# Kernel tuning notes

Measured on AMD Instinct MI355X. Metric: run time of the kernel, lower is better.

## Reference

```python
import jax, jax.numpy as jnp
import numpy as np
import math

B, H, W = 4, 224, 224
NFEAT = 2048
N_SP, N_FAM, N_ORD = 200, 38, 13
THRESH = 0.5


def _conv(x, w, b, s):
    y = jax.lax.conv_general_dilated(x, w, (s, s), 'SAME', dimension_numbers=('NCHW', 'OIHW', 'NCHW'))
    return y + b[None, :, None, None]


def _features(x, bw1, bb1, bw2, bb2, bw3, bb3, bw4, bb4):
    # stride-32 CNN backbone standing in for nn.Sequential(*model.children()[:-2]) (2048-ch output)
    x = jax.nn.relu(_conv(x, bw1, bb1, 4))
    x = jax.nn.relu(_conv(x, bw2, bb2, 2))
    x = jax.nn.relu(_conv(x, bw3, bb3, 2))
    x = jax.nn.relu(_conv(x, bw4, bb4, 2))
    return x


def _resize_ac(img, y1, y2, x1, x2, oh, ow):
    # bilinear, align_corners=True resample of img[:, y1:y2, x1:x2] -> (C, oh, ow); jit-safe (gather, no dynamic shapes)
    Hh, Ww = img.shape[1], img.shape[2]
    ys = y1 + jnp.arange(oh, dtype=jnp.float32) * (y2 - 1 - y1) / (oh - 1)
    xs = x1 + jnp.arange(ow, dtype=jnp.float32) * (x2 - 1 - x1) / (ow - 1)
    ylo = jnp.clip(jnp.floor(ys).astype(jnp.int32), 0, Hh - 1)
    yhi = jnp.clip(ylo + 1, 0, Hh - 1)
    yf = (ys - ylo)[None, :, None]
    rows = img[:, ylo, :] * (1 - yf) + img[:, yhi, :] * yf
    xlo = jnp.clip(jnp.floor(xs).astype(jnp.int32), 0, Ww - 1)
    xhi = jnp.clip(xlo + 1, 0, Ww - 1)
    xf = (xs - xlo)[None, None, :]
    return rows[:, :, xlo] * (1 - xf) + rows[:, :, xhi] * xf


def _obj_loc(score, threshold):
    # vectorized, sync-free version of the torch obj_loc interval search
    n = score.shape[0]
    minsize = int(math.ceil(n * 0.125))
    defmax = int(math.ceil(n * 0.875))
    snorm = jnp.sign(score - threshold)
    cross = jnp.abs(snorm[1:] - snorm[:-1]) == 2  # crossing between j and j+1 -> index j+1 starts... torch puts index j in next interval
    ind = jnp.concatenate([cross, jnp.zeros((1,), bool)]).astype(jnp.int32)
    seg = jnp.cumsum(ind)  # segment id per position; matches torch half-open intervals [p_i, p_{i+1})
    k = jnp.sum(ind)       # number of crossings
    idx = jnp.arange(n, dtype=jnp.int32)
    seg_max = jax.ops.segment_max(score, seg, num_segments=n)
    seg_len = jax.ops.segment_sum(jnp.ones((n,), jnp.int32), seg, num_segments=n)
    seg_start = jax.ops.segment_min(idx, seg, num_segments=n)
    seg_end = jax.ops.segment_max(idx, seg, num_segments=n) + 1
    valid = (idx <= k) & (seg_len > 0)
    # torch processing order: first interval, then last, then interiors; ties keep earlier-processed
    order = jnp.where(idx == 0, 0, jnp.where(idx == k, 1, idx + 1))
    m = jnp.where(valid, seg_max, -jnp.inf)
    c1 = valid & (m == jnp.max(m))
    best_len = jnp.max(jnp.where(c1, seg_len, -1))
    c2 = c1 & (seg_len == best_len)
    sel = jnp.argmin(jnp.where(c2, order, n + 2))
    zmin, zmax = seg_start[sel], seg_end[sel]
    # min-size padding, exactly mirroring the sequential torch ifs
    pad = minsize - (zmax - zmin)
    hp = (pad + 1) // 2  # ceil(pad/2)
    need = (zmax - zmin) <= minsize
    cA = need & (zmin > hp) & (n - zmax > pad)
    zmin = jnp.where(cA, zmin - hp + 1, zmin)
    zmax = jnp.where(cA, zmax + hp, zmax)
    cB = need & (zmin < hp)
    zmin = jnp.where(cB, 0, zmin)
    zmax = jnp.where(cB, minsize, zmax)
    cC = need & (n - zmax < hp)
    zmin = jnp.where(cC, n - minsize + 1, zmin)
    zmax = jnp.where(cC, n, zmax)
    # no crossings -> fixed central window (torch early return)
    zmin = jnp.where(k == 0, minsize, zmin)
    zmax = jnp.where(k == 0, defmax, zmax)
    return zmin, zmax


def _norm01(v):
    mn, mx = v.min(), v.max()
    den = jnp.where(mx == mn, mx, mx - mn)
    num = jnp.where(mx == mn, v, v - mn)
    return num / den


def _w_h(gs, wscore, hscore, inputs, threshold):
    def one(g, wsc, hsc, img):
        top = jnp.argmax(g)  # == sort(descending)[0]
        x1, x2 = _obj_loc(_norm01(wsc[top]), threshold)
        y1, y2 = _obj_loc(_norm01(hsc[top]), threshold)
        return _resize_ac(img, y1, y2, x1, x2, img.shape[1], img.shape[2])
    return jax.vmap(one)(gs, wscore, hscore, inputs)


def _stage(gvec, fmap, inputs, wc, bc, wc1, bc1, lf_prev, bb):
    gf = gvec @ wc.T + bc  # conv1x1 on pooled feature == linear
    cam = jax.nn.sigmoid(jnp.einsum('bchw,oc->bohw', jax.lax.stop_gradient(fmap), wc) + bc[None, :, None, None])
    fh, fw = fmap.shape[2], fmap.shape[3]
    cam_up = jax.vmap(lambda im: _resize_ac(im, 0, fh, 0, fw, H, W))(cam)  # (B,C,H,W)
    wsc = cam_up.max(axis=2)  # max_pool2d((h,1)) -> (B,C,W)
    hsc = cam_up.max(axis=3)  # max_pool2d((1,w)) -> (B,C,H)
    lin = _w_h(gf, wsc, hsc, inputs, THRESH)
    la = _features(jax.lax.stop_gradient(lin), *bb)
    lf = la.mean(axis=(2, 3))  # AdaptiveAvgPool2d(1)
    ls = lf @ wc1.T + bc1
    if lf_prev is not None:
        ls = ls + (lf_prev @ wc1.T + bc1)  # bias added twice, as in torch
    return (gf + ls) / 2.0, lf


def _forward(inputs, bw1, bb1, bw2, bb2, bw3, bb3, bw4, bb4, w_ord, b_ord, w_ord1, b_ord1, w_fam, b_fam, w_fam1, b_fam1, w_sp, b_sp, w_sp1, b_sp1):
    bb = (bw1, bb1, bw2, bb2, bw3, bb3, bw4, bb4)
    fmap = _features(inputs, *bb)
    gvec = fmap.mean(axis=(2, 3))
    f_ord, lf_ord = _stage(gvec, fmap, inputs, w_ord, b_ord, w_ord1, b_ord1, None, bb)
    f_fam, lf_fam = _stage(gvec, fmap, inputs, w_fam, b_fam, w_fam1, b_fam1, lf_ord, bb)
    f_sp, _ = _stage(gvec, fmap, inputs, w_sp, b_sp, w_sp1, b_sp1, lf_fam, bb)
    return f_sp, f_fam, f_ord


def setup_inputs() -> dict:
    ks = jax.random.split(jax.random.key(0), 16)
    def he(k, shape, fan_in):
        return jax.random.normal(k, shape, jnp.float32) * np.float32(np.sqrt(2.0 / fan_in))
    d = {"inputs": jax.random.normal(ks[0], (B, 3, H, W), jnp.float32)}
    d["bw1"], d["bb1"] = he(ks[1], (256, 3, 7, 7), 3 * 49), jnp.zeros((256,), jnp.float32)
    d["bw2"], d["bb2"] = he(ks[2], (512, 256, 3, 3), 256 * 9), jnp.zeros((512,), jnp.float32)
    d["bw3"], d["bb3"] = he(ks[3], (1024, 512, 1, 1), 512), jnp.zeros((1024,), jnp.float32)
    d["bw4"], d["bb4"] = he(ks[4], (2048, 1024, 1, 1), 1024), jnp.zeros((2048,), jnp.float32)
    for i, (nm, nc) in enumerate([("ord", N_ORD), ("fam", N_FAM), ("sp", N_SP)]):
        d["w_" + nm] = he(ks[5 + 2 * i], (nc, NFEAT), NFEAT)
        d["b_" + nm] = jnp.zeros((nc,), jnp.float32)
        d["w_" + nm + "1"] = he(ks[6 + 2 * i], (nc, NFEAT), NFEAT)
        d["b_" + nm + "1"] = jnp.zeros((nc,), jnp.float32)
    return d


def reference(inputs, bw1, bb1, bw2, bb2, bw3, bb3, bw4, bb4, w_ord, b_ord, w_ord1, b_ord1, w_fam, b_fam, w_fam1, b_fam1, w_sp, b_sp, w_sp1, b_sp1):
    return _forward(inputs, bw1, bb1, bw2, bb2, bw3, bb3, bw4, bb4, w_ord, b_ord, w_ord1, b_ord1, w_fam, b_fam, w_fam1, b_fam1, w_sp, b_sp, w_sp1, b_sp1)
```

## Files before the change

### kernel.cpp

```cpp
#include <hip/hip_runtime.h>
#include <hip/hip_bf16.h>
#include <math.h>

#define TPB 256

typedef __attribute__((ext_vector_type(8))) short s16x8;
typedef __attribute__((ext_vector_type(8))) unsigned short u16x8;
typedef __attribute__((ext_vector_type(4))) float f32x4;

__global__ void conv3x3s2_k(const float* __restrict__ in, const float* __restrict__ w,
                            const float* __restrict__ bias, float* __restrict__ out, int N)
{
  int bid = blockIdx.x;
  if (N == 4) {
    const int xcd = bid & 7;
    const int n_img = xcd >> 1;
    const int kk = ((bid >> 3) << 1) | (xcd & 1);
    bid = n_img * 392 + kk;
  }
  int idx = bid * blockDim.x + threadIdx.x;
  int total = N * 512 * 28 * 7;
  if (idx >= total) return;
  int oxg = idx % 7; int t = idx / 7; int oy = t % 28; t /= 28; int oc = t % 512; int n = t / 512;
  const float* inp = in + (size_t)n * 256 * 3136;
  const float* wp = w + (size_t)oc * 2304;
  float b0 = bias[oc];
  float acc0 = b0, acc1 = b0, acc2 = b0, acc3 = b0;
  int xb0 = oxg * 8;
  #pragma unroll 4
  for (int ic = 0; ic < 256; ic++) {
    const float* ich = inp + (size_t)ic * 3136;
    const float* wr = wp + ic * 9;
    #pragma unroll
    for (int ky = 0; ky < 3; ky++) {
      int iy = oy * 2 + ky;
      if (iy >= 56) continue;
      const float* row = ich + iy * 56;
      float w0 = wr[ky * 3 + 0], w1 = wr[ky * 3 + 1], w2 = wr[ky * 3 + 2];
      {
        int xb = xb0 + 0;
        acc0 += row[xb] * w0 + row[xb + 1] * w1 + row[xb + 2] * w2;
      }
      {
        int xb = xb0 + 2;
        acc1 += row[xb] * w0 + row[xb + 1] * w1 + row[xb + 2] * w2;
      }
      {
        int xb = xb0 + 4;
        acc2 += row[xb] * w0 + row[xb + 1] * w1 + row[xb + 2] * w2;
      }
      {
        int xb = xb0 + 6;
        acc3 += row[xb] * w0 + row[xb + 1] * w1;
        if (xb + 2 < 56) acc3 += row[xb + 2] * w2;
      }
    }
  }
  float* op = out + (((size_t)n * 512 + oc) * 28 + oy) * 28 + oxg * 4;
  op[0] = fmaxf(acc0, 0.f);
  op[1] = fmaxf(acc1, 0.f);
  op[2] = fmaxf(acc2, 0.f);
  op[3] = fmaxf(acc3, 0.f);
}

template<int KH, int KW, int STRIDE, int PADL, bool BINIT>
__global__ __launch_bounds__(256)
void conv_igemm_k(const float* __restrict__ in, const float* __restrict__ w,
                  const float* __restrict__ bias, float* __restrict__ out,
                  int Cin, int Cout, int Hin, int OH, int Np, int K)
{
  __shared__ float As[16][136];
  __shared__ float Bs[16][64];

  const int tid = threadIdx.x;
  const int bx = blockIdx.x;
  const int by = blockIdx.y;
  const int OHW = OH * OH;
  const int HinHin = Hin * Hin;

  const int n_sub = tid & 63;
  const int kq = tid >> 6;
  const int n_g = bx * 64 + n_sub;
  const bool nvalid = (n_g < Np);
  const int n_c = nvalid ? n_g : 0;
  const int img = n_c / OHW;
  const int p = n_c - img * OHW;
  const int oy = p / OH;
  const int ox = p - oy * OH;
  const int iy0 = oy * STRIDE - PADL;
  const int ix0 = ox * STRIDE - PADL;
  const float* inb = in + (size_t)img * Cin * HinHin;

  const int ks = tid & 15;
  const int msq = tid >> 4;
  const int m_base = by * 128;

  const int m0 = (tid >> 4) * 8;
  const int n0 = (tid & 15) * 4;

  float acc[8][4];
  #pragma unroll
  for (int i = 0; i < 8; i++) {
    const float init = BINIT ? bias[m_base + m0 + i] : 0.f;
    #pragma unroll
    for (int j = 0; j < 4; j++) acc[i][j] = init;
  }

  const int KT = (K + 15) >> 4;
  for (int kt = 0; kt < KT; kt++) {
    const int k0 = kt * 16;
    #pragma unroll
    for (int j = 0; j < 8; j++) {
      const int m = msq + 16 * j;
      const int k = k0 + ks;
      float v = 0.f;
      if (k < K) v = w[(size_t)(m_base + m) * K + k];
      As[ks][m] = v;
    }
    #pragma unroll
    for (int j = 0; j < 4; j++) {
      const int k = k0 + kq * 4 + j;
      float v = 0.f;
      if (nvalid && k < K) {
        const int c = k / (KH * KW);
        const int r = k - c * (KH * KW);
        const int ky = r / KW;
        const int kx = r - ky * KW;
        const int iy = iy0 + ky;
        const int ix = ix0 + kx;
        if (iy >= 0 && iy < Hin && ix >= 0 && ix < Hin)
          v = inb[(size_t)c * HinHin + iy * Hin + ix];
      }
      Bs[kq * 4 + j][n_sub] = v;
    }
    __syncthreads();
    #pragma unroll
    for (int k = 0; k < 16; k++) {
      float a_[8], b_[4];
      #pragma unroll
      for (int i = 0; i < 8; i++) a_[i] = As[k][m0 + i];
      #pragma unroll
      for (int j = 0; j < 4; j++) b_[j] = Bs[k][n0 + j];
      #pragma unroll
      for (int i = 0; i < 8; i++)
        #pragma unroll
        for (int j = 0; j < 4; j++) acc[i][j] += a_[i] * b_[j];
    }
    __syncthreads();
  }

  #pragma unroll
  for (int i = 0; i < 8; i++) {
    const int m = m_base + m0 + i;
    const float bv = BINIT ? 0.f : bias[m];
    #pragma unroll
    for (int j = 0; j < 4; j++) {
      const int nn = bx * 64 + n0 + j;
      if (nn < Np) {
        const int img2 = nn / OHW;
        const int pp = nn - img2 * OHW;
        const float v = BINIT ? acc[i][j] : (acc[i][j] + bv);
        out[((size_t)img2 * Cout + m) * OHW + pp] = fmaxf(v, 0.f);
      }
    }
  }
}

__global__ __launch_bounds__(256)
void conv1x1_igemm32_k(const float* __restrict__ in, const float* __restrict__ w,
                       const float* __restrict__ bias, float* __restrict__ out,
                       int Cin, int Cout, int Hin, int OH, int Np)
{
  __shared__ float As[32][33];
  __shared__ float Bs[32][65];

  const int tid = threadIdx.x;
  const int bx = blockIdx.x;
  const int by = blockIdx.y;
  const int OHW = OH * OH;
  const int HH = Hin * Hin;
  const int m_base = by * 32;

  const int am = tid >> 3;
  const int ak0 = (tid & 7) * 4;
  const int bk = tid >> 3;
  const int bn0 = (tid & 7) * 8;
  const int cn = tid & 63;
  const int cm0 = (tid >> 6) * 8;
  const int n_g = bx * 64 + cn;

  float acc[8];
  #pragma unroll
  for (int i = 0; i < 8; i++) acc[i] = bias[m_base + cm0 + i];

  int bpix[8]; bool bval[8];
  #pragma unroll
  for (int j = 0; j < 8; j++) {
    int n = bx * 64 + bn0 + j;
    bval[j] = (n < Np);
    int nn = bval[j] ? n : 0;
    int img = nn / OHW; int pp = nn - img * OHW; int oy = pp / OH; int ox = pp - oy * OH;
    bpix[j] = img * Cin * HH + (2 * oy) * Hin + 2 * ox;
  }

  for (int k0 = 0; k0 < Cin; k0 += 32) {
    #pragma unroll
    for (int j = 0; j < 4; j++)
      As[ak0 + j][am] = w[(size_t)(m_base + am) * Cin + k0 + ak0 + j];
    #pragma unroll
    for (int j = 0; j < 8; j++)
      Bs[bk][bn0 + j] = bval[j] ? in[(size_t)(k0 + bk) * HH + bpix[j]] : 0.f;
    __syncthreads();
    #pragma unroll
    for (int k = 0; k < 32; k++) {
      float b = Bs[k][cn];
      #pragma unroll
      for (int i = 0; i < 8; i++) acc[i] += As[k][cm0 + i] * b;
    }
    __syncthreads();
  }

  if (n_g < Np) {
    int img = n_g / OHW; int pp = n_g - img * OHW;
    #pragma unroll
    for (int i = 0; i < 8; i++)
      out[((size_t)img * Cout + m_base + cm0 + i) * OHW + pp] = fmaxf(acc[i], 0.f);
  }
}

__global__ void cvt_bf16_k(const float* __restrict__ in, unsigned short* __restrict__ out, int n)
{
  int i = blockIdx.x * blockDim.x + threadIdx.x;
  if (i >= n) return;
  __hip_bfloat16 h = __float2bfloat16(in[i]);
  out[i] = *reinterpret_cast<unsigned short*>(&h);
}

__global__ void cvt_bf16_pad_k(const float* __restrict__ in, unsigned short* __restrict__ out,
                               int rows, int kin, int kout)
{
  int i = blockIdx.x * blockDim.x + threadIdx.x;
  if (i >= rows * kout) return;
  int r = i / kout, k = i - r * kout;
  unsigned short v = 0;
  if (k < kin) {
    __hip_bfloat16 h = __float2bfloat16(in[(size_t)r * kin + k]);
    v = *reinterpret_cast<unsigned short*>(&h);
  }
  out[i] = v;
}

template<int KH, int KW, int STRIDE, int PADL>
__global__ __launch_bounds__(256)
void conv_mfma_k(const float* __restrict__ in, const unsigned short* __restrict__ wbf,
                 const float* __restrict__ bias, float* __restrict__ out,
                 int Cin, int Cout, int Hin, int OH, int Np, int K, int kreal)
{
  __shared__ unsigned short As[64 * 40];
  __shared__ unsigned short Bs[64 * 40];

  const int tid = threadIdx.x;
  const int bx = blockIdx.x;
  const int by = blockIdx.y;
  const int OHW = OH * OH;
  const int HH = Hin * Hin;
  const int m_base = by * 64;

  const int n_sub = tid & 63;
  const int kq = tid >> 6;
  const int n_g = bx * 64 + n_sub;
  const bool nv = (n_g < Np);
  const int n_c = nv ? n_g : 0;
  const int img = n_c / OHW;
  const int p = n_c - img * OHW;
  const int oy = p / OH;
  const int ox = p - oy * OH;
  const int iy0 = oy * STRIDE - PADL;
  const int ix0 = ox * STRIDE - PADL;
  const float* inb = in + (size_t)img * Cin * HH;

  const int arow = tid >> 2;
  const int akoff = (tid & 3) * 8;

  const int wv = tid >> 6;
  const int ln = tid & 63;
  const int lr = ln & 15;
  const int lq = ln >> 4;

  f32x4 acc[4];
  #pragma unroll
  for (int nf = 0; nf < 4; nf++) acc[nf] = (f32x4){0.f, 0.f, 0.f, 0.f};

#define GATHER_TILE(K0, AV, BV)                                                   \
  {                                                                               \
    AV = *(const u16x8*)(wbf + (size_t)(m_base + arow) * K + (K0) + akoff);       \
    _Pragma("unroll")                                                             \
    for (int i = 0; i < 8; i++) {                                                 \
      const int k = (K0) + kq * 8 + i;                                            \
      float v = 0.f;                                                              \
      if (nv && k < kreal) {                                                      \
        const int c = k / (KH * KW);                                              \
        const int r = k - c * (KH * KW);                                          \
        const int ky = r / KW;                                                    \
        const int kx = r - ky * KW;                                               \
        const int iy = iy0 + ky;                                                  \
        const int ix = ix0 + kx;                                                  \
        if (iy >= 0 && iy < Hin && ix >= 0 && ix < Hin)                           \
          v = inb[(size_t)c * HH + iy * Hin + ix];                                \
      }                                                                           \
      __hip_bfloat16 h = __float2bfloat16(v);                                     \
      BV[i] = *reinterpret_cast<unsigned short*>(&h);                             \
    }                                                                             \
  }

  u16x8 av, bv;
  GATHER_TILE(0, av, bv);

  for (int k0 = 0; k0 < K; k0 += 32) {
    *(u16x8*)&As[arow * 40 + akoff] = av;
    *(u16x8*)&Bs[n_sub * 40 + kq * 8] = bv;
    __syncthreads();

    if (k0 + 32 < K) { GATHER_TILE(k0 + 32, av, bv); }

    s16x8 a = *(const s16x8*)&As[(wv * 16 + lr) * 40 + lq * 8];
    #pragma unroll
    for (int nf = 0; nf < 4; nf++) {
      s16x8 b = *(const s16x8*)&Bs[(nf * 16 + lr) * 40 + lq * 8];
      acc[nf] = __builtin_amdgcn_mfma_f32_16x16x32_bf16(a, b, acc[nf], 0, 0, 0);
    }
    __syncthreads();
  }
#undef GATHER_TILE

  #pragma unroll
  for (int nf = 0; nf < 4; nf++) {
    const int n_gl = bx * 64 + nf * 16 + lr;
    if (n_gl < Np) {
      const int img2 = n_gl / OHW;
      const int pp = n_gl - img2 * OHW;
      #pragma unroll
      for (int r = 0; r < 4; r++) {
        const int m = m_base + wv * 16 + lq * 4 + r;
        out[((size_t)img2 * Cout + m) * OHW + pp] = fmaxf(acc[nf][r] + bias[m], 0.f);
      }
    }
  }
}

__global__ void pool_k(const float* __restrict__ in, float* __restrict__ out, int total)
{
  int idx = blockIdx.x * blockDim.x + threadIdx.x;
  if (idx >= total) return;
  const float* p = in + (size_t)idx * 49;
  float s = 0.f;
  #pragma unroll
  for (int i = 0; i < 49; i++) s += p[i];
  out[idx] = s / 49.f;
}

__global__ void gf_k(const float* __restrict__ gvec,
                     const float* __restrict__ w_ord, const float* __restrict__ b_ord,
                     const float* __restrict__ w_fam, const float* __restrict__ b_fam,
                     const float* __restrict__ w_sp,  const float* __restrict__ b_sp,
                     float* __restrict__ gfbuf)
{
  int idx = blockIdx.x * blockDim.x + threadIdx.x;
  if (idx >= 12 * 256) return;
  int o = idx % 256; int t = idx / 256; int b = t % 4; int s = t / 4;
  int nc = (s == 0) ? 13 : ((s == 1) ? 38 : 200);
  if (o >= nc) return;
  const float* w = (s == 0) ? w_ord : ((s == 1) ? w_fam : w_sp);
  const float* bb = (s == 0) ? b_ord : ((s == 1) ? b_fam : b_sp);
  float acc = bb[o];
  const float* g = gvec + (size_t)b * 2048;
  const float* wr = w + (size_t)o * 2048;
  for (int c = 0; c < 2048; c++) acc += g[c] * wr[c];
  gfbuf[idx] = acc;
}

__device__ void obj_loc_dev(const float* sc, int* zmin_o, int* zmax_o)
{
  const int n = 224, minsize = 28, defmax = 196;
  float mn = sc[0], mx = sc[0];
  for (int i = 1; i < n; i++) { mn = fminf(mn, sc[i]); mx = fmaxf(mx, sc[i]); }
  float den = (mx == mn) ? mx : (mx - mn);
#define NV(i) (((mx == mn) ? sc[i] : (sc[i] - mn)) / den)
#define SGN(v) (((v) > 0.5f) ? 1 : (((v) < 0.5f) ? -1 : 0))

  int k = 0; float M = -INFINITY;
  {
    float v = NV(0); int sg = SGN(v);
    float smax = -INFINITY; int cnt = 0;
    for (int j = 0; j < n; j++) {
      int indj = 0; float vn = 0.f; int sgn_nx = 0;
      if (j < n - 1) { vn = NV(j + 1); sgn_nx = SGN(vn); int d = sgn_nx - sg; indj = (d == 2 || d == -2); }
      if (indj) { if (cnt > 0) M = fmaxf(M, smax); k++; smax = -INFINITY; cnt = 0; }
      smax = fmaxf(smax, v); cnt++;
      if (j < n - 1) { v = vn; sg = sgn_nx; }
    }
    if (cnt > 0) M = fmaxf(M, smax);
  }

  int zmin, zmax;
  if (k == 0) { zmin = minsize; zmax = defmax; }
  else {
    int bestlen = -1;
    {
      float v = NV(0); int sg = SGN(v);
      float smax = -INFINITY; int cnt = 0;
      for (int j = 0; j < n; j++) {
        int indj = 0; float vn = 0.f; int sgn_nx = 0;
        if (j < n - 1) { vn = NV(j + 1); sgn_nx = SGN(vn); int d = sgn_nx - sg; indj = (d == 2 || d == -2); }
        if (indj) { if (cnt > 0 && smax == M && cnt > bestlen) bestlen = cnt; smax = -INFINITY; cnt = 0; }
        smax = fmaxf(smax, v); cnt++;
        if (j < n - 1) { v = vn; sg = sgn_nx; }
      }
      if (cnt > 0 && smax == M && cnt > bestlen) bestlen = cnt;
    }
    int bestorder = 1 << 30; int bzmin = 0, bzmax = 0;
    {
      float v = NV(0); int sg = SGN(v);
      float smax = -INFINITY; int cnt = 0; int start = 0; int sid = 0;
      for (int j = 0; j < n; j++) {
        int indj = 0; float vn = 0.f; int sgn_nx = 0;
        if (j < n - 1) { vn = NV(j + 1); sgn_nx = SGN(vn); int d = sgn_nx - sg; indj = (d == 2 || d == -2); }
        if (indj) {
          if (cnt > 0 && smax == M && cnt == bestlen) {
            int order = (sid == 0) ? 0 : ((sid == k) ? 1 : (sid + 1));
            if (order < bestorder) { bestorder = order; bzmin = start; bzmax = j; }
          }
          sid++; start = j; smax = -INFINITY; cnt = 0;
        }
        smax = fmaxf(smax, v); cnt++;
        if (j < n - 1) { v = vn; sg = sgn_nx; }
      }
      if (cnt > 0 && smax == M && cnt == bestlen) {
        int order = (sid == 0) ? 0 : ((sid == k) ? 1 : (sid + 1));
        if (order < bestorder) { bestorder = order; bzmin = start; bzmax = n; }
      }
    }
    zmin = bzmin; zmax = bzmax;
    int pad = minsize - (zmax - zmin);
    int hp = (pad + 1) / 2;
    int need = ((zmax - zmin) <= minsize);
    if (need && (zmin > hp) && ((n - zmax) > pad)) { zmin = zmin - hp + 1; zmax = zmax + hp; }
    if (need && (zmin < hp)) { zmin = 0; zmax = minsize; }
    if (need && ((n - zmax) < hp)) { zmin = n - minsize + 1; zmax = n; }
  }
  *zmin_o = zmin; *zmax_o = zmax;
#undef NV
#undef SGN
}

__global__ void cam_k(const float* __restrict__ fmap,
                      const float* __restrict__ gfbuf,
                      const float* __restrict__ w_ord, const float* __restrict__ b_ord,
                      const float* __restrict__ w_fam, const float* __restrict__ b_fam,
                      const float* __restrict__ w_sp,  const float* __restrict__ b_sp,
                      int* __restrict__ crops)
{
  int bid = blockIdx.x;
  int s = bid / 4, b = bid % 4;
  int nc = (s == 0) ? 13 : ((s == 1) ? 38 : 200);
  const float* wc = (s == 0) ? w_ord : ((s == 1) ? w_fam : w_sp);
  const float* bc = (s == 0) ? b_ord : ((s == 1) ? b_fam : b_sp);

  __shared__ float cam7[49];
  __shared__ float wsc[224];
  __shared__ float hsc[224];
  __shared__ int top_s;
  int tid = threadIdx.x;

  if (tid == 0) {
    const float* g = gfbuf + (size_t)bid * 256;
    int best = 0; float bv = g[0];
    for (int i = 1; i < nc; i++) { if (g[i] > bv) { bv = g[i]; best = i; } }
    top_s = best;
  }
  __syncthreads();
  int top = top_s;

  if (tid < 49) {
    const float* fp = fmap + (size_t)b * 2048 * 49 + tid;
    const float* wr = wc + (size_t)top * 2048;
    float acc = bc[top];
    for (int c = 0; c < 2048; c++) acc += fp[(size_t)c * 49] * wr[c];
    cam7[tid] = 1.f / (1.f + expf(-acc));
  }
  __syncthreads();

  if (tid < 224) {
    {
      int xx = tid;
      float xsf = (float)(xx * 6) / 223.f;
      int xlo = (int)floorf(xsf); if (xlo > 6) xlo = 6; if (xlo < 0) xlo = 0;
      int xhi = xlo + 1; if (xhi > 6) xhi = 6;
      float xf = xsf - (float)xlo;
      float m = -INFINITY;
      for (int yy = 0; yy < 224; yy++) {
        float ysf = (float)(yy * 6) / 223.f;
        int ylo = (int)floorf(ysf); if (ylo > 6) ylo = 6; if (ylo < 0) ylo = 0;
        int yhi = ylo + 1; if (yhi > 6) yhi = 6;
        float yf = ysf - (float)ylo;
        float r0 = cam7[ylo * 7 + xlo] * (1.f - yf) + cam7[yhi * 7 + xlo] * yf;
        float r1 = cam7[ylo * 7 + xhi] * (1.f - yf) + cam7[yhi * 7 + xhi] * yf;
        m = fmaxf(m, r0 * (1.f - xf) + r1 * xf);
      }
      wsc[xx] = m;
    }
    {
      int yy = tid;
      float ysf = (float)(yy * 6) / 223.f;
      int ylo = (int)floorf(ysf); if (ylo > 6) ylo = 6; if (ylo < 0) ylo = 0;
      int yhi = ylo + 1; if (yhi > 6) yhi = 6;
      float yf = ysf - (float)ylo;
      float m = -INFINITY;
      for (int xx = 0; xx < 224; xx++) {
        float xsf = (float)(xx * 6) / 223.f;
        int xlo = (int)floorf(xsf); if (xlo > 6) xlo = 6; if (xlo < 0) xlo = 0;
        int xhi = xlo + 1; if (xhi > 6) xhi = 6;
        float xf = xsf - (float)xlo;
        float r0 = cam7[ylo * 7 + xlo] * (1.f - yf) + cam7[yhi * 7 + xlo] * yf;
        float r1 = cam7[ylo * 7 + xhi] * (1.f - yf) + cam7[yhi * 7 + xhi] * yf;
        m = fmaxf(m, r0 * (1.f - xf) + r1 * xf);
      }
      hsc[yy] = m;
    }
  }
  __syncthreads();

  if (tid == 0) {
    int zmin, zmax; obj_loc_dev(wsc, &zmin, &zmax);
    crops[bid * 4 + 0] = zmin; crops[bid * 4 + 1] = zmax;
  } else if (tid == 1) {
    int zmin, zmax; obj_loc_dev(hsc, &zmin, &zmax);
    crops[bid * 4 + 2] = zmin; crops[bid * 4 + 3] = zmax;
  }
}

__global__ void crop_resize_k(const float* __restrict__ in, const int* __restrict__ crops,
                              float* __restrict__ lin)
{
  int idx = blockIdx.x * blockDim.x + threadIdx.x;
  int total = 12 * 3 * 224 * 224;
  if (idx >= total) return;
  int xx = idx % 224; int t = idx / 224; int yy = t % 224; t /= 224; int c = t % 3; int img = t / 3;
  int b = img % 4;
  int x1 = crops[img * 4 + 0], x2 = crops[img * 4 + 1];
  int y1 = crops[img * 4 + 2], y2 = crops[img * 4 + 3];
  float ys = (float)y1 + (float)(yy * (y2 - 1 - y1)) / 223.f;
  float xs = (float)x1 + (float)(xx * (x2 - 1 - x1)) / 223.f;
  int ylo = (int)floorf(ys); if (ylo < 0) ylo = 0; if (ylo > 223) ylo = 223;
  int yhi = ylo + 1; if (yhi > 223) yhi = 223;
  float yf = ys - (float)ylo;
  int xlo = (int)floorf(xs); if (xlo < 0) xlo = 0; if (xlo > 223) xlo = 223;
  int xhi = xlo + 1; if (xhi > 223) xhi = 223;
  float xf = xs - (float)xlo;
  const float* im = in + ((size_t)b * 3 + c) * 50176;
  float r0 = im[ylo * 224 + xlo] * (1.f - yf) + im[yhi * 224 + xlo] * yf;
  float r1 = im[ylo * 224 + xhi] * (1.f - yf) + im[yhi * 224 + xhi] * yf;
  lin[idx] = r0 * (1.f - xf) + r1 * xf;
}

__global__ __launch_bounds__(64)
void final_v2_k(const float* __restrict__ lf12,
                const float* __restrict__ gfbuf,
                const float* __restrict__ w_ord1, const float* __restrict__ b_ord1,
                const float* __restrict__ w_fam1, const float* __restrict__ b_fam1,
                const float* __restrict__ w_sp1,  const float* __restrict__ b_sp1,
                float* __restrict__ out)
{
  int id = blockIdx.x;
  if (id >= 1004) return;
  int s, b, o; const float *w1, *b1;
  if (id < 800)      { s = 2; o = id % 200;        b = id / 200;        w1 = w_sp1;  b1 = b_sp1; }
  else if (id < 952) { s = 1; o = (id-800) % 38;   b = (id-800) / 38;   w1 = w_fam1; b1 = b_fam1; }
  else               { s = 0; o = (id-952) % 13;   b = (id-952) / 13;   w1 = w_ord1; b1 = b_ord1; }
  const int lane = threadIdx.x;
  const float* wr = w1 + (size_t)o * 2048;
  const float* lfc = lf12 + (size_t)(s * 4 + b) * 2048;
  float p1 = 0.f, p2 = 0.f;
  for (int c = lane; c < 2048; c += 64) p1 = fmaf(lfc[c], wr[c], p1);
  if (s > 0) {
    const float* lfp = lf12 + (size_t)((s - 1) * 4 + b) * 2048;
    for (int c = lane; c < 2048; c += 64) p2 = fmaf(lfp[c], wr[c], p2);
  }
  #pragma unroll
  for (int off = 32; off > 0; off >>= 1) {
    p1 += __shfl_down(p1, off);
    p2 += __shfl_down(p2, off);
  }
  if (lane == 0) {
    float ls = b1[o] + p1;
    if (s > 0) ls += b1[o] + p2;
    out[id] = (gfbuf[(size_t)(s * 4 + b) * 256 + o] + ls) * 0.5f;
  }
}


static inline int nblk(long long total) { return (int)((total + TPB - 1) / TPB); }
static inline int ntile(int total, int t) { return (total + t - 1) / t; }

extern "C" void kernel_launch(void* const* d_in, const int* in_sizes, int n_in,
                              void* d_out, int out_size, void* d_ws, size_t ws_size,
                              hipStream_t stream)
{
  const float* inputs = (const float*)d_in[0];
  const float* bw1 = (const float*)d_in[1];  const float* bb1 = (const float*)d_in[2];
  const float* bw2 = (const float*)d_in[3];  const float* bb2 = (const float*)d_in[4];
  const float* bw3 = (const float*)d_in[5];  const float* bb3 = (const float*)d_in[6];
  const float* bw4 = (const float*)d_in[7];  const float* bb4 = (const float*)d_in[8];
  const float* w_ord  = (const float*)d_in[9];   const float* b_ord  = (const float*)d_in[10];
  const float* w_ord1 = (const float*)d_in[11];  const float* b_ord1 = (const float*)d_in[12];
  const float* w_fam  = (const float*)d_in[13];  const float* b_fam  = (const float*)d_in[14];
  const float* w_fam1 = (const float*)d_in[15];  const float* b_fam1 = (const float*)d_in[16];
  const float* w_sp   = (const float*)d_in[17];  const float* b_sp   = (const float*)d_in[18];
  const float* w_sp1  = (const float*)d_in[19];  const float* b_sp1  = (const float*)d_in[20];
  float* out = (float*)d_out;

  float* ws = (float*)d_ws;
  size_t o_x1 = 0;
  size_t o_x2 = o_x1 + (size_t)12 * 256 * 3136;
  size_t o_x3 = o_x2 + (size_t)12 * 512 * 784;
  size_t o_x4 = o_x3 + (size_t)12 * 1024 * 196;
  size_t o_gvec = o_x4 + (size_t)12 * 2048 * 49;
  size_t o_gf = o_gvec + 4 * 2048;
  size_t o_lf = o_gf + 12 * 256;
  size_t o_crop = o_lf + 12 * 2048;
  size_t o_wbf1 = o_crop + 64;
  float* x1 = ws + o_x1;
  float* x2 = ws + o_x2;
  float* x3 = ws + o_x3;
  float* x4 = ws + o_x4;
  float* gvec = ws + o_gvec;
  float* gfbuf = ws + o_gf;
  float* lf12 = ws + o_lf;
  int* crops = (int*)(ws + o_crop);
  float* lin = ws + o_x2;
  unsigned short* wbf1 = (unsigned short*)(ws + o_wbf1);
  unsigned short* wbf2 = (unsigned short*)x3;
  unsigned short* wbf3 = (unsigned short*)x4;
  unsigned short* wbf4 = (unsigned short*)x1;

  cvt_bf16_pad_k<<<nblk(256 * 160), TPB, 0, stream>>>(bw1, wbf1, 256, 147, 160);

  {
    int np1 = 4 * 56 * 56;
    conv_igemm_k<7,7,4,1,true><<<dim3(ntile(np1,64), 2), 256, 0, stream>>>(inputs, bw1, bb1, x1, 3, 256, 224, 56, np1, 147);
    conv3x3s2_k<<<nblk((long long)4 * 512 * 28 * 7), TPB, 0, stream>>>(x1, bw2, bb2, x2, 4);
    int np3 = 4 * 14 * 14;
    conv1x1_igemm32_k<<<dim3(ntile(np3,64), 32), 256, 0, stream>>>(x2, bw3, bb3, x3, 512, 1024, 28, 14, np3);
    int np4 = 4 * 7 * 7;
    conv1x1_igemm32_k<<<dim3(ntile(np4,64), 64), 256, 0, stream>>>(x3, bw4, bb4, x4, 1024, 2048, 14, 7, np4);
  }
  pool_k<<<nblk(4 * 2048), TPB, 0, stream>>>(x4, gvec, 4 * 2048);

  gf_k<<<nblk(12 * 256), TPB, 0, stream>>>(gvec, w_ord, b_ord, w_fam, b_fam, w_sp, b_sp, gfbuf);
  cam_k<<<12, TPB, 0, stream>>>(x4, gfbuf, w_ord, b_ord, w_fam, b_fam, w_sp, b_sp, crops);
  crop_resize_k<<<nblk((long long)12 * 3 * 224 * 224), TPB, 0, stream>>>(inputs, crops, lin);

  {
    int np1 = 12 * 56 * 56;
    conv_mfma_k<7,7,4,1><<<dim3(588, 4), 256, 0, stream>>>(lin, wbf1, bb1, x1, 3, 256, 224, 56, np1, 160, 147);

    cvt_bf16_k<<<nblk(512 * 2304), TPB, 0, stream>>>(bw2, wbf2, 512 * 2304);
    int np2 = 12 * 28 * 28;
    conv_mfma_k<3,3,2,0><<<dim3(147, 8), 256, 0, stream>>>(x1, wbf2, bb2, x2, 256, 512, 56, 28, np2, 2304, 2304);

    cvt_bf16_k<<<nblk(1024 * 512), TPB, 0, stream>>>(bw3, wbf3, 1024 * 512);
    int np3 = 12 * 14 * 14;
    conv_mfma_k<1,1,2,0><<<dim3(ntile(np3,64), 16), 256, 0, stream>>>(x2, wbf3, bb3, x3, 512, 1024, 28, 14, np3, 512, 512);

    cvt_bf16_k<<<nblk(2048 * 1024), TPB, 0, stream>>>(bw4, wbf4, 2048 * 1024);
    int np4 = 12 * 7 * 7;
    conv_mfma_k<1,1,2,0><<<dim3(ntile(np4,64), 32), 256, 0, stream>>>(x3, wbf4, bb4, x4, 1024, 2048, 14, 7, np4, 1024, 1024);
  }
  pool_k<<<nblk(12 * 2048), TPB, 0, stream>>>(x4, lf12, 12 * 2048);

  final_v2_k<<<1004, 64, 0, stream>>>(lf12, gfbuf, w_ord1, b_ord1, w_fam1, b_fam1, w_sp1, b_sp1, out);
}
```

Measured before the change: 2.098 ms.

## Widen MFMA conv tile to 128 output channels and remap fp32 3x3 conv threads

New measurement: 2.001 ms. -4.6%, faster.

```diff
diff --git a/kernel.cpp b/kernel.cpp
--- a/kernel.cpp
+++ b/kernel.cpp
@@ -8,20 +8,22 @@
 typedef __attribute__((ext_vector_type(8))) unsigned short u16x8;
 typedef __attribute__((ext_vector_type(4))) float f32x4;
 
-__global__ void conv3x3s2_k(const float* __restrict__ in, const float* __restrict__ w,
-                            const float* __restrict__ bias, float* __restrict__ out, int N)
-{
-  int bid = blockIdx.x;
-  if (N == 4) {
-    const int xcd = bid & 7;
-    const int n_img = xcd >> 1;
-    const int kk = ((bid >> 3) << 1) | (xcd & 1);
-    bid = n_img * 392 + kk;
-  }
-  int idx = bid * blockDim.x + threadIdx.x;
-  int total = N * 512 * 28 * 7;
-  if (idx >= total) return;
-  int oxg = idx % 7; int t = idx / 7; int oy = t % 28; t /= 28; int oc = t % 512; int n = t / 512;
+__global__ void conv3x3s2_r0_k(const float* __restrict__ in, const float* __restrict__ w,
+                               const float* __restrict__ bias, float* __restrict__ out)
+{
+  const int d = blockIdx.x;
+  const int xcd = d & 7;
+  const int n = xcd & 3;
+  const int ipair = ((d >> 3) << 1) | (xcd >> 2);
+  const int wave = ipair * 4 + (threadIdx.x >> 6);
+  const int oct = wave % 57;
+  const int oy = wave / 57;
+  const int lane = threadIdx.x & 63;
+  const int oc_low = lane / 7;
+  const int oxg = lane - oc_low * 7;
+  const int oc = oct * 9 + oc_low;
+  if (oc_low > 8 || oc >= 512) return;
+
   const float* inp = in + (size_t)n * 256 * 3136;
   const float* wp = w + (size_t)oc * 2304;
   float b0 = bias[oc];
@@ -252,11 +254,11 @@
 
 template<int KH, int KW, int STRIDE, int PADL>
 __global__ __launch_bounds__(256)
-void conv_mfma_k(const float* __restrict__ in, const unsigned short* __restrict__ wbf,
-                 const float* __restrict__ bias, float* __restrict__ out,
-                 int Cin, int Cout, int Hin, int OH, int Np, int K, int kreal)
-{
-  __shared__ unsigned short As[64 * 40];
+void conv_mfma2_k(const float* __restrict__ in, const unsigned short* __restrict__ wbf,
+                  const float* __restrict__ bias, float* __restrict__ out,
+                  int Cin, int Cout, int Hin, int OH, int Np, int K, int kreal)
+{
+  __shared__ unsigned short As[128 * 40];
   __shared__ unsigned short Bs[64 * 40];
 
   const int tid = threadIdx.x;
@@ -264,7 +266,7 @@
   const int by = blockIdx.y;
   const int OHW = OH * OH;
   const int HH = Hin * Hin;
-  const int m_base = by * 64;
+  const int m_base = by * 128;
 
   const int n_sub = tid & 63;
   const int kq = tid >> 6;
@@ -279,21 +281,28 @@
   const int ix0 = ox * STRIDE - PADL;
   const float* inb = in + (size_t)img * Cin * HH;
 
-  const int arow = tid >> 2;
-  const int akoff = (tid & 3) * 8;
+  const int arow = tid >> 1;
+  const int akoff = (tid & 1) * 16;
 
   const int wv = tid >> 6;
   const int ln = tid & 63;
   const int lr = ln & 15;
   const int lq = ln >> 4;
 
-  f32x4 acc[4];
-  #pragma unroll
-  for (int nf = 0; nf < 4; nf++) acc[nf] = (f32x4){0.f, 0.f, 0.f, 0.f};
-
-#define GATHER_TILE(K0, AV, BV)                                                   \
+  f32x4 acc[2][4];
+  #pragma unroll
+  for (int h = 0; h < 2; h++)
+    #pragma unroll
+    for (int nf = 0; nf < 4; nf++) acc[h][nf] = (f32x4){0.f, 0.f, 0.f, 0.f};
+
+#define GATHER_A(K0, A0, A1)                                                      \
   {                                                                               \
-    AV = *(const u16x8*)(wbf + (size_t)(m_base + arow) * K + (K0) + akoff);       \
+    const unsigned short* wr_ = wbf + (size_t)(m_base + arow) * K + (K0) + akoff; \
+    A0 = *(const u16x8*)(wr_);                                                    \
+    A1 = *(const u16x8*)(wr_ + 8);                                                \
+  }
+#define GATHER_B(K0, BV)                                                          \
+  {                                                                               \
     _Pragma("unroll")                                                             \
     for (int i = 0; i < 8; i++) {                                                 \
       const int k = (K0) + kq * 8 + i;                                            \
@@ -308,41 +317,49 @@
         if (iy >= 0 && iy < Hin && ix >= 0 && ix < Hin)                           \
           v = inb[(size_t)c * HH + iy * Hin + ix];                                \
       }                                                                           \
-      __hip_bfloat16 h = __float2bfloat16(v);                                     \
-      BV[i] = *reinterpret_cast<unsigned short*>(&h);                             \
+      __hip_bfloat16 h_ = __float2bfloat16(v);                                    \
+      BV[i] = *reinterpret_cast<unsigned short*>(&h_);                            \
     }                                                                             \
   }
 
-  u16x8 av, bv;
-  GATHER_TILE(0, av, bv);
+  u16x8 a0, a1, bv;
+  GATHER_A(0, a0, a1);
+  GATHER_B(0, bv);
 
   for (int k0 = 0; k0 < K; k0 += 32) {
-    *(u16x8*)&As[arow * 40 + akoff] = av;
+    *(u16x8*)&As[arow * 40 + akoff] = a0;
+    *(u16x8*)&As[arow * 40 + akoff + 8] = a1;
     *(u16x8*)&Bs[n_sub * 40 + kq * 8] = bv;
     __syncthreads();
 
-    if (k0 + 32 < K) { GATHER_TILE(k0 + 32, av, bv); }
-
-    s16x8 a = *(const s16x8*)&As[(wv * 16 + lr) * 40 + lq * 8];
+    if (k0 + 32 < K) { GATHER_A(k0 + 32, a0, a1); GATHER_B(k0 + 32, bv); }
+
+    s16x8 am0 = *(const s16x8*)&As[(wv * 16 + lr) * 40 + lq * 8];
+    s16x8 am1 = *(const s16x8*)&As[(64 + wv * 16 + lr) * 40 + lq * 8];
     #pragma unroll
     for (int nf = 0; nf < 4; nf++) {
       s16x8 b = *(const s16x8*)&Bs[(nf * 16 + lr) * 40 + lq * 8];
-      acc[nf] = __builtin_amdgcn_mfma_f32_16x16x32_bf16(a, b, acc[nf], 0, 0, 0);
+      acc[0][nf] = __builtin_amdgcn_mfma_f32_16x16x32_bf16(am0, b, acc[0][nf], 0, 0, 0);
+      acc[1][nf] = __builtin_amdgcn_mfma_f32_16x16x32_bf16(am1, b, acc[1][nf], 0, 0, 0);
     }
     __syncthreads();
   }
-#undef GATHER_TILE
-
-  #pragma unroll
-  for (int nf = 0; nf < 4; nf++) {
-    const int n_gl = bx * 64 + nf * 16 + lr;
-    if (n_gl < Np) {
-      const int img2 = n_gl / OHW;
-      const int pp = n_gl - img2 * OHW;
-      #pragma unroll
-      for (int r = 0; r < 4; r++) {
-        const int m = m_base + wv * 16 + lq * 4 + r;
-        out[((size_t)img2 * Cout + m) * OHW + pp] = fmaxf(acc[nf][r] + bias[m], 0.f);
+#undef GATHER_A
+#undef GATHER_B
+
+  #pragma unroll
+  for (int h = 0; h < 2; h++) {
+    #pragma unroll
+    for (int nf = 0; nf < 4; nf++) {
+      const int n_gl = bx * 64 + nf * 16 + lr;
+      if (n_gl < Np) {
+        const int img2 = n_gl / OHW;
+        const int pp = n_gl - img2 * OHW;
+        #pragma unroll
+        for (int r = 0; r < 4; r++) {
+          const int m = m_base + h * 64 + wv * 16 + lq * 4 + r;
+          out[((size_t)img2 * Cout + m) * OHW + pp] = fmaxf(acc[h][nf][r] + bias[m], 0.f);
+        }
       }
     }
   }
@@ -648,7 +665,7 @@
   {
     int np1 = 4 * 56 * 56;
     conv_igemm_k<7,7,4,1,true><<<dim3(ntile(np1,64), 2), 256, 0, stream>>>(inputs, bw1, bb1, x1, 3, 256, 224, 56, np1, 147);
-    conv3x3s2_k<<<nblk((long long)4 * 512 * 28 * 7), TPB, 0, stream>>>(x1, bw2, bb2, x2, 4);
+    conv3x3s2_r0_k<<<1596, 256, 0, stream>>>(x1, bw2, bb2, x2);
     int np3 = 4 * 14 * 14;
     conv1x1_igemm32_k<<<dim3(ntile(np3,64), 32), 256, 0, stream>>>(x2, bw3, bb3, x3, 512, 1024, 28, 14, np3);
     int np4 = 4 * 7 * 7;
@@ -662,19 +679,19 @@
 
   {
     int np1 = 12 * 56 * 56;
-    conv_mfma_k<7,7,4,1><<<dim3(588, 4), 256, 0, stream>>>(lin, wbf1, bb1, x1, 3, 256, 224, 56, np1, 160, 147);
+    conv_mfma2_k<7,7,4,1><<<dim3(588, 2), 256, 0, stream>>>(lin, wbf1, bb1, x1, 3, 256, 224, 56, np1, 160, 147);
 
     cvt_bf16_k<<<nblk(512 * 2304), TPB, 0, stream>>>(bw2, wbf2, 512 * 2304);
     int np2 = 12 * 28 * 28;
-    conv_mfma_k<3,3,2,0><<<dim3(147, 8), 256, 0, stream>>>(x1, wbf2, bb2, x2, 256, 512, 56, 28, np2, 2304, 2304);
+    conv_mfma2_k<3,3,2,0><<<dim3(147, 4), 256, 0, stream>>>(x1, wbf2, bb2, x2, 256, 512, 56, 28, np2, 2304, 2304);
 
     cvt_bf16_k<<<nblk(1024 * 512), TPB, 0, stream>>>(bw3, wbf3, 1024 * 512);
     int np3 = 12 * 14 * 14;
-    conv_mfma_k<1,1,2,0><<<dim3(ntile(np3,64), 16), 256, 0, stream>>>(x2, wbf3, bb3, x3, 512, 1024, 28, 14, np3, 512, 512);
+    conv_mfma2_k<1,1,2,0><<<dim3(ntile(np3,64), 8), 256, 0, stream>>>(x2, wbf3, bb3, x3, 512, 1024, 28, 14, np3, 512, 512);
 
     cvt_bf16_k<<<nblk(2048 * 1024), TPB, 0, stream>>>(bw4, wbf4, 2048 * 1024);
     int np4 = 12 * 7 * 7;
-    conv_mfma_k<1,1,2,0><<<dim3(ntile(np4,64), 32), 256, 0, stream>>>(x3, wbf4, bb4, x4, 1024, 2048, 14, 7, np4, 1024, 1024);
+    conv_mfma2_k<1,1,2,0><<<dim3(ntile(np4,64), 16), 256, 0, stream>>>(x3, wbf4, bb4, x4, 1024, 2048, 14, 7, np4, 1024, 1024);
   }
   pool_k<<<nblk(12 * 2048), TPB, 0, stream>>>(x4, lf12, 12 * 2048);
 
```
